# Kernel optimization log

Measured on AMD Instinct MI355X. Metric: run time of the kernel, lower is better.

Reference implementation:

```python
import jax, jax.numpy as jnp
import numpy as np

B, N, C_SA, OUT = 16, 2048, 512, 1024
BN_EPS = 1e-5


def pconv(x, w, b=None):
    # 1x1 Conv1d: x [B,Cin,N], w [Cout,Cin] -> [B,Cout,N]
    y = jnp.einsum('oc,bcn->bon', w, x)
    return y if b is None else y + b[None, :, None]


def setup_inputs() -> dict:
    key = jax.random.key(0)
    ks = jax.random.split(key, 16)
    s = lambda k, shape: jax.random.normal(k, shape, dtype=jnp.float32) * 0.05
    return {
        'x': jax.random.normal(ks[0], (B, 3, N), dtype=jnp.float32),
        'w1': s(ks[1], (128, 21)), 'b1': s(ks[2], (128,)),
        'w2': s(ks[3], (256, 128)), 'b2': s(ks[4], (256,)),
        'w3': s(ks[5], (512, 512)), 'b3': s(ks[6], (512,)),
        'w4': s(ks[7], (OUT, 512)), 'b4': s(ks[8], (OUT,)),
        'wqk': s(ks[9], (C_SA // 4, C_SA)),            # q_conv.weight tied to k_conv.weight, no bias
        'wv': s(ks[10], (C_SA, C_SA)), 'bv': s(ks[11], (C_SA,)),
        'wt': s(ks[12], (C_SA, C_SA)), 'bt': s(ks[13], (C_SA,)),
        'gamma': jnp.ones((C_SA,), dtype=jnp.float32),
        'beta': jnp.zeros((C_SA,), dtype=jnp.float32),
    }


def reference(x, w1, b1, w2, b2, w3, b3, w4, b4, wqk, wv, bv, wt, bt, gamma, beta):
    b, _, n = x.shape
    # positional encoding on [B,N,3]: [t, sin(t*2^i), cos(t*2^i)] for i in 0..2 -> 21 channels
    t = jnp.transpose(x, (0, 2, 1))
    enc = [t]
    for f in (1.0, 2.0, 4.0):
        enc.append(jnp.sin(t * f))
        enc.append(jnp.cos(t * f))
    h = jnp.transpose(jnp.concatenate(enc, axis=-1), (0, 2, 1))  # [B,21,N]

    h = jax.nn.relu(pconv(h, w1, b1))               # [B,128,N]
    h = pconv(h, w2, b2)                            # [B,256,N]
    g = jnp.max(h, axis=2)                          # [B,256]
    h = jnp.concatenate([h, jnp.broadcast_to(g[:, :, None], (b, g.shape[1], n))], axis=1)  # [B,512,N]
    h = jax.nn.relu(pconv(h, w3, b3))               # [B,512,N]

    # SA_Layer (offset attention, double normalization)
    xq = jnp.einsum('oc,bcn->bno', wqk, h)          # [B,N,128]
    xk = jnp.einsum('oc,bcn->bon', wqk, h)          # [B,128,N]
    xv = pconv(h, wv, bv)                           # [B,512,N]
    energy = jnp.einsum('bqo,bok->bqk', xq, xk)     # [B,N,N]
    attn = jax.nn.softmax(energy, axis=-1)
    attn = attn / (1e-9 + jnp.sum(attn, axis=1, keepdims=True))  # L1 renorm over query dim
    x_r = jnp.einsum('bck,bqk->bcq', xv, attn)      # x_v @ attn^T -> [B,512,N]
    d = pconv(h - x_r, wt, bt)
    # BatchNorm1d, training mode (batch statistics, biased variance)
    mu = jnp.mean(d, axis=(0, 2))
    var = jnp.var(d, axis=(0, 2))
    d = gamma[None, :, None] * (d - mu[None, :, None]) * jax.lax.rsqrt(var + BN_EPS)[None, :, None] + beta[None, :, None]
    h = h + jax.nn.relu(d)

    h = pconv(h, w4, b4)                            # [B,OUT,N]
    return jnp.max(h, axis=2)                       # [B,OUT]
```

## Files before the change

### kernel.cpp

```cpp
#include <hip/hip_runtime.h>
#include <cmath>

#define GN 2048
#define GB 16

typedef __attribute__((ext_vector_type(8))) short bf8_t;
typedef __attribute__((ext_vector_type(4))) float f4_t;

__device__ __forceinline__ short f2bf(float f) {
    union { float f; unsigned u; } v; v.f = f;
    unsigned r = v.u + 0x7FFFu + ((v.u >> 16) & 1u);
    return (short)(r >> 16);
}
__device__ __forceinline__ float bf2f(short s) {
    union { unsigned u; float f; } v; v.u = ((unsigned)(unsigned short)s) << 16;
    return v.f;
}

__device__ __forceinline__ void load16_lds(const short* g, short* l) {
    __builtin_amdgcn_global_load_lds(
        (const __attribute__((address_space(1))) unsigned int*)g,
        (__attribute__((address_space(3))) unsigned int*)l, 16, 0, 0);
}

__device__ __forceinline__ float wave_max(float v) {
#pragma unroll
    for (int o = 32; o > 0; o >>= 1) v = fmaxf(v, __shfl_xor(v, o, 64));
    return v;
}
__device__ __forceinline__ float wave_sum(float v) {
#pragma unroll
    for (int o = 32; o > 0; o >>= 1) v += __shfl_xor(v, o, 64);
    return v;
}
__device__ __forceinline__ float block_sum(float v) {
    __shared__ float sm[4];
    v = wave_sum(v);
    if ((threadIdx.x & 63) == 0) sm[threadIdx.x >> 6] = v;
    __syncthreads();
    v = sm[0] + sm[1] + sm[2] + sm[3];
    __syncthreads();
    return v;
}

__global__ __launch_bounds__(256) void f2ball_k(
    const float* __restrict__ w2, const float* __restrict__ w3,
    const float* __restrict__ wqk, const float* __restrict__ wv,
    const float* __restrict__ wt, const float* __restrict__ w4,
    short* __restrict__ dst) {
    int i = blockIdx.x * 256 + threadIdx.x;
    if (i >= 1409024) return;
    float v;
    if (i < 32768) v = w2[i];
    else if (i < 294912) v = w3[i - 32768];
    else if (i < 360448) v = wqk[i - 294912];
    else if (i < 622592) v = wv[i - 360448];
    else if (i < 884736) v = wt[i - 622592];
    else v = w4[i - 884736];
    dst[i] = f2bf(v);
}

__global__ __launch_bounds__(256) void posenc_conv1_k(
    const float* __restrict__ x, const float* __restrict__ w1,
    const float* __restrict__ b1, short* __restrict__ h1) {
    __shared__ float w[128 * 21];
    __shared__ float bb[128];
    __shared__ float se[256][21];
    const int tid = threadIdx.x;
    for (int i = tid; i < 128 * 21; i += 256) w[i] = w1[i];
    if (tid < 128) bb[tid] = b1[tid];
    int p0 = blockIdx.x * 256;
    int p = p0 + tid, b = p >> 11, n = p & (GN - 1);
    const float* xb = x + (long)b * 3 * GN + n;
    float t0 = xb[0], t1 = xb[GN], t2 = xb[2 * GN];
    se[tid][0] = t0; se[tid][1] = t1; se[tid][2] = t2;
    se[tid][3] = sinf(t0); se[tid][4] = sinf(t1); se[tid][5] = sinf(t2);
    se[tid][6] = cosf(t0); se[tid][7] = cosf(t1); se[tid][8] = cosf(t2);
    se[tid][9] = sinf(2.f * t0); se[tid][10] = sinf(2.f * t1); se[tid][11] = sinf(2.f * t2);
    se[tid][12] = cosf(2.f * t0); se[tid][13] = cosf(2.f * t1); se[tid][14] = cosf(2.f * t2);
    se[tid][15] = sinf(4.f * t0); se[tid][16] = sinf(4.f * t1); se[tid][17] = sinf(4.f * t2);
    se[tid][18] = cosf(4.f * t0); se[tid][19] = cosf(4.f * t1); se[tid][20] = cosf(4.f * t2);
    __syncthreads();
    short* outb = h1 + (long)p0 * 128;
    for (int it = 0; it < 128; ++it) {
        int L = it * 256 + tid;
        int pl = L >> 7, o = L & 127;
        float s = bb[o];
        const float* er = se[pl];
        const float* wr = &w[o * 21];
#pragma unroll
        for (int c = 0; c < 21; ++c) s = fmaf(wr[c], er[c], s);
        outb[L] = f2bf(fmaxf(s, 0.f));
    }
}

template <int MODE, int BIAS, bool RELU, bool STATS = false, bool COLMAX = false>
__global__ __launch_bounds__(256) void mm_k(
    const short* __restrict__ A, int lda, long long aB,
    const short* __restrict__ B, int ldb, long long bB,
    const float* __restrict__ bias, int biasStride,
    const short* __restrict__ aux, long long auxB,
    const float* __restrict__ rsv,
    float* __restrict__ Cf, long long cfB,
    short* __restrict__ Cb, long long cbB,
    float* __restrict__ Pmax, float* __restrict__ Ps2,
    int ldc, int K) {
    const int z = blockIdx.z;
    A += (long long)z * aB;
    B += (long long)z * bB;
    if (MODE == 4) { aux += (long long)z * auxB; rsv += (long long)z * GN; }
    if (MODE == 1) Cf += (long long)z * cfB;
    if (MODE == 2 || MODE == 4 || MODE == 6) Cb += (long long)z * cbB;
    if (MODE == 6) Pmax += (long long)z * GN * 32;
    const int row0 = blockIdx.x * 128, col0 = blockIdx.y * 128;
    const int tid = threadIdx.x;
    const int lane = tid & 63, w = tid >> 6;
    const int r = lane & 15, q = lane >> 4;
    const int wr = w >> 1, wc = w & 1;

    __shared__ short lA[8192];
    __shared__ short lB[8192];

    f4_t acc[4][4] = {};

    const int sRow = lane >> 2;
    const int sKb = (lane & 3) ^ ((lane >> 3) & 3);
    const long aG = (long)(row0 + w * 32 + sRow) * lda + sKb * 8;
    const long bG = (long)(col0 + w * 32 + sRow) * ldb + sKb * 8;
    short* ldsA0 = lA + (w * 32) * 32;
    short* ldsA1 = lA + (w * 32 + 16) * 32;
    short* ldsB0 = lB + (w * 32) * 32;
    short* ldsB1 = lB + (w * 32 + 16) * 32;

    const int sw = (q ^ ((r >> 1) & 3)) * 8;
    int aoff[4], boff[4];
#pragma unroll
    for (int i = 0; i < 4; ++i) {
        aoff[i] = (wr * 64 + i * 16 + r) * 32 + sw;
        boff[i] = (wc * 64 + i * 16 + r) * 32 + sw;
    }

    for (int k0 = 0; k0 < K; k0 += 64) {
        __syncthreads();
        load16_lds(A + aG + k0, ldsA0);
        load16_lds(A + aG + (long)16 * lda + k0, ldsA1);
        load16_lds(B + bG + k0, ldsB0);
        load16_lds(B + bG + (long)16 * ldb + k0, ldsB1);
        load16_lds(A + aG + k0 + 32, ldsA0 + 4096);
        load16_lds(A + aG + (long)16 * lda + k0 + 32, ldsA1 + 4096);
        load16_lds(B + bG + k0 + 32, ldsB0 + 4096);
        load16_lds(B + bG + (long)16 * ldb + k0 + 32, ldsB1 + 4096);
        asm volatile("s_waitcnt vmcnt(0)" ::: "memory");
        __syncthreads();
#pragma unroll
        for (int h = 0; h < 2; ++h) {
            const short* la = lA + h * 4096;
            const short* lb = lB + h * 4096;
            bf8_t av[4], bv[4];
#pragma unroll
            for (int i = 0; i < 4; ++i) av[i] = *(const bf8_t*)(la + aoff[i]);
#pragma unroll
            for (int j = 0; j < 4; ++j) bv[j] = *(const bf8_t*)(lb + boff[j]);
#pragma unroll
            for (int i = 0; i < 4; ++i)
#pragma unroll
                for (int j = 0; j < 4; ++j)
                    acc[i][j] = __builtin_amdgcn_mfma_f32_16x16x32_bf16(av[i], bv[j], acc[i][j], 0, 0, 0);
        }
    }

    if constexpr (MODE == 5) {
        int b = row0 >> 11;
        int rw = (blockIdx.x * 2 + wr) & 31;
#pragma unroll
        for (int j = 0; j < 4; ++j) {
            float vm = -1e30f;
#pragma unroll
            for (int i = 0; i < 4; ++i)
#pragma unroll
                for (int e = 0; e < 4; ++e) vm = fmaxf(vm, acc[i][j][e]);
            vm = fmaxf(vm, __shfl_xor(vm, 16, 64));
            vm = fmaxf(vm, __shfl_xor(vm, 32, 64));
            if (q == 0) {
                int gcol = col0 + wc * 64 + j * 16 + r;
                Pmax[(((long)b * 1024 + gcol) << 5) + rw] = vm + bias[gcol];
            }
        }
    } else if constexpr (MODE == 6) {
        float rsum[4][4] = {};
#pragma unroll
        for (int j = 0; j < 4; ++j) {
            int gcol = col0 + wc * 64 + j * 16 + r;
#pragma unroll
            for (int i = 0; i < 4; ++i) {
#pragma unroll
                for (int e = 0; e < 4; ++e) {
                    int grow = row0 + wr * 64 + i * 16 + q * 4 + e;
                    float ex = __expf(acc[i][j][e]);
                    rsum[i][e] += ex;
                    Cb[(long)grow * ldc + gcol] = f2bf(ex);
                }
            }
        }
#pragma unroll
        for (int i = 0; i < 4; ++i)
#pragma unroll
            for (int e = 0; e < 4; ++e) {
                float v = rsum[i][e];
                v += __shfl_xor(v, 1, 64);
                v += __shfl_xor(v, 2, 64);
                v += __shfl_xor(v, 4, 64);
                v += __shfl_xor(v, 8, 64);
                if (r == 0) {
                    int grow = row0 + wr * 64 + i * 16 + q * 4 + e;
                    Pmax[((long)grow << 5) + blockIdx.y * 2 + wc] = v;
                }
            }
    } else if constexpr (MODE == 4) {
#pragma unroll
        for (int i = 0; i < 4; ++i) {
#pragma unroll
            for (int e = 0; e < 4; ++e) {
                int grow = row0 + wr * 64 + i * 16 + q * 4 + e;
                float rsr = rsv[grow];
                long ob = (long)grow * ldc + col0 + wc * 64 + r;
#pragma unroll
                for (int j = 0; j < 4; ++j) {
                    long off = ob + j * 16;
                    Cb[off] = f2bf(bf2f(aux[off]) - acc[i][j][e] * rsr);
                }
            }
        }
    } else {
        const int b2d = (BIAS == 3) ? (row0 >> 11) : 0;
#pragma unroll
        for (int j = 0; j < 4; ++j) {
            int gcol = col0 + wc * 64 + j * 16 + r;
            float bvv = 0.f;
            if constexpr (BIAS == 1) bvv = bias[gcol];
            if constexpr (BIAS == 3) bvv = bias[b2d * biasStride + gcol];
            float s1 = 0.f, s2 = 0.f;
            float cmx = -1e30f;
#pragma unroll
            for (int i = 0; i < 4; ++i) {
#pragma unroll
                for (int e = 0; e < 4; ++e) {
                    int grow = row0 + wr * 64 + i * 16 + q * 4 + e;
                    float v = acc[i][j][e] + bvv;
                    if constexpr (BIAS == 2) v += bias[grow];
                    if constexpr (RELU) v = fmaxf(v, 0.f);
                    if constexpr (STATS) { s1 += v; s2 = fmaf(v, v, s2); }
                    if constexpr (COLMAX) cmx = fmaxf(cmx, v);
                    long off = (long)grow * ldc + gcol;
                    if constexpr (MODE == 1) Cf[off] = v;
                    if constexpr (MODE == 2) Cb[off] = f2bf(v);
                }
            }
            if constexpr (STATS) {
                s1 += __shfl_xor(s1, 16, 64); s1 += __shfl_xor(s1, 32, 64);
                s2 += __shfl_xor(s2, 16, 64); s2 += __shfl_xor(s2, 32, 64);
                if (q == 0) {
                    int rw2 = blockIdx.x * 2 + wr;
                    Pmax[rw2 * 512 + gcol] = s1;
                    Ps2[rw2 * 512 + gcol] = s2;
                }
            }
            if constexpr (COLMAX) {
                cmx = fmaxf(cmx, __shfl_xor(cmx, 16, 64));
                cmx = fmaxf(cmx, __shfl_xor(cmx, 32, 64));
                if (q == 0) {
                    int b = row0 >> 11;
                    int rw = (blockIdx.x * 2 + wr) & 31;
                    Pmax[(((long)b * ldc + gcol) << 5) + rw] = cmx;
                }
            }
        }
    }
}

__device__ __forceinline__ void stage2(const short* g0, const short* g1, short* dst) {
    load16_lds(g0, dst);
    load16_lds(g1, dst + 4096);
}

template <int MH, int NH>
__device__ __forceinline__ void mfma_quad(const bf8_t (&av)[4][2], const bf8_t (&bv)[2][2],
                                          f4_t (&acc)[8][4]) {
#pragma unroll
    for (int mi = 0; mi < 4; ++mi)
#pragma unroll
        for (int ni = 0; ni < 2; ++ni) {
            acc[MH * 4 + mi][NH * 2 + ni] = __builtin_amdgcn_mfma_f32_16x16x32_bf16(
                av[mi][0], bv[ni][0], acc[MH * 4 + mi][NH * 2 + ni], 0, 0, 0);
            acc[MH * 4 + mi][NH * 2 + ni] = __builtin_amdgcn_mfma_f32_16x16x32_bf16(
                av[mi][1], bv[ni][1], acc[MH * 4 + mi][NH * 2 + ni], 0, 0, 0);
        }
}

__device__ __forceinline__ void rd4(const short* p, int swz0, int swz1, bf8_t (&v)[4][2]) {
#pragma unroll
    for (int i = 0; i < 4; ++i) {
        v[i][0] = *(const bf8_t*)(p + i * 1024 + swz0);
        v[i][1] = *(const bf8_t*)(p + i * 1024 + swz1);
    }
}
__device__ __forceinline__ void rd2(const short* p, int swz0, int swz1, bf8_t (&v)[2][2]) {
#pragma unroll
    for (int i = 0; i < 2; ++i) {
        v[i][0] = *(const bf8_t*)(p + i * 1024 + swz0);
        v[i][1] = *(const bf8_t*)(p + i * 1024 + swz1);
    }
}

#define SB0 __builtin_amdgcn_sched_barrier(0)
#define BARRIER asm volatile("s_barrier" ::: "memory")

template <int MODE, int BIAS, bool RELU, bool STATS = false>
__global__ __launch_bounds__(512, 2) void mm256_k(
    const short* __restrict__ A, int lda, long long aB,
    const short* __restrict__ B, int ldb, long long bB,
    const float* __restrict__ bias,
    const short* __restrict__ aux, long long auxB,
    const float* __restrict__ rsv,
    short* __restrict__ Cb, long long cbB,
    float* __restrict__ Pmax, float* __restrict__ Ps2,
    int ldc, int K) {
    __shared__ short lA[32768];
    __shared__ short lB[32768];
    const int z = blockIdx.z;
    A += (long long)z * aB;
    B += (long long)z * bB;
    if constexpr (MODE == 4) { aux += (long long)z * auxB; rsv += (long long)z * GN; }
    if constexpr (MODE != 5) Cb += (long long)z * cbB;
    const int row0 = blockIdx.x * 256, col0 = blockIdx.y * 256;
    const int tid = threadIdx.x;
    const int lane = tid & 63, w = tid >> 6;
    const int r16 = lane & 15, q = lane >> 4;
    const int wr = w >> 2, wc = w & 3;

    const int rc0 = w * 8 + (lane >> 3);
    const int s8 = ((lane & 7) ^ (rc0 & 7)) * 8;
    const long ldA64 = (long)64 * lda, ldB64 = (long)64 * ldb;
    const short* aH0 = A + (long)(row0 + rc0) * lda + s8;
    const short* aH1 = aH0 + (long)128 * lda;
    const short* bH0 = B + (long)(col0 + rc0) * ldb + s8;
    const short* bH1 = bH0 + (long)128 * ldb;
    short* dA = lA + w * 512;
    short* dB = lB + w * 512;

#define STG_A(d_, h_, kt_) stage2((h_ ? aH1 : aH0) + (long)(kt_) * 64,                      \
                                  (h_ ? aH1 : aH0) + (long)(kt_) * 64 + ldA64,              \
                                  dA + (d_) * 16384 + (h_) * 8192)
#define STG_B(d_, h_, kt_) stage2((h_ ? bH1 : bH0) + (long)(kt_) * 64,                      \
                                  (h_ ? bH1 : bH0) + (long)(kt_) * 64 + ldB64,              \
                                  dB + (d_) * 16384 + (h_) * 8192)

    const int swz0 = (q ^ (r16 & 7)) * 8;
    const int swz1 = ((4 + q) ^ (r16 & 7)) * 8;
    const int arow = (wr * 64 + r16) * 64;
    const int brow = (wc * 32 + r16) * 64;

    f4_t acc[8][4] = {};
    bf8_t av[4][2], bv0[2][2], bv1[2][2];
    const int NT = K >> 6;

    STG_A(0, 0, 0); STG_B(0, 0, 0); STG_B(0, 1, 0); STG_A(0, 1, 0);
    STG_A(1, 0, 1); STG_B(1, 0, 1);
    asm volatile("s_waitcnt vmcnt(4)" ::: "memory");
    SB0; BARRIER; SB0;

    for (int t = 0; t < NT; ++t) {
        const int d = t & 1;
        const short* la = lA + d * 16384;
        const short* lb = lB + d * 16384;
        rd4(la + arow, swz0, swz1, av);
        rd2(lb + brow, swz0, swz1, bv0);
        if (t + 1 < NT) STG_B(d ^ 1, 1, t + 1);
        SB0; BARRIER; SB0;
        __builtin_amdgcn_s_setprio(1);
        mfma_quad<0, 0>(av, bv0, acc);
        __builtin_amdgcn_s_setprio(0);
        SB0; BARRIER; SB0;
        rd2(lb + 8192 + brow, swz0, swz1, bv1);
        if (t + 1 < NT) STG_A(d ^ 1, 1, t + 1);
        SB0; BARRIER; SB0;
        __builtin_amdgcn_s_setprio(1);
        mfma_quad<0, 1>(av, bv1, acc);
        __builtin_amdgcn_s_setprio(0);
        SB0; BARRIER; SB0;
        rd4(la + 8192 + arow, swz0, swz1, av);
        if (t + 2 < NT) STG_A(d, 0, t + 2);
        SB0; BARRIER; SB0;
        __builtin_amdgcn_s_setprio(1);
        mfma_quad<1, 0>(av, bv0, acc);
        __builtin_amdgcn_s_setprio(0);
        SB0; BARRIER; SB0;
        if (t + 2 < NT) {
            STG_B(d, 0, t + 2);
            asm volatile("s_waitcnt vmcnt(4)" ::: "memory");
        } else if (t + 1 < NT) {
            asm volatile("s_waitcnt vmcnt(0)" ::: "memory");
        }
        SB0; BARRIER; SB0;
        __builtin_amdgcn_s_setprio(1);
        mfma_quad<1, 1>(av, bv1, acc);
        __builtin_amdgcn_s_setprio(0);
        SB0; BARRIER; SB0;
    }
#undef STG_A
#undef STG_B

    const int mrow = row0 + wr * 64 + q * 4;
    const int ncol = col0 + wc * 32 + r16;

    if constexpr (MODE == 4) {
#pragma unroll
        for (int m = 0; m < 8; ++m) {
#pragma unroll
            for (int e = 0; e < 4; ++e) {
                const int grow = mrow + (m >> 2) * 128 + (m & 3) * 16 + e;
                const float rsr = rsv[grow];
                const long rb = (long)grow * ldc;
#pragma unroll
                for (int n = 0; n < 4; ++n) {
                    const long off = rb + ncol + (n >> 1) * 128 + (n & 1) * 16;
                    Cb[off] = f2bf(bf2f(aux[off]) - acc[m][n][e] * rsr);
                }
            }
        }
    } else if constexpr (MODE == 2) {
#pragma unroll
        for (int n = 0; n < 4; ++n) {
            const int gcol = ncol + (n >> 1) * 128 + (n & 1) * 16;
            float bvv = 0.f;
            if constexpr (BIAS == 1) bvv = bias[gcol];
#pragma unroll
            for (int mh = 0; mh < 2; ++mh) {
                float s1 = 0.f, s2 = 0.f;
#pragma unroll
                for (int mi = 0; mi < 4; ++mi) {
#pragma unroll
                    for (int e = 0; e < 4; ++e) {
                        const int grow = mrow + mh * 128 + mi * 16 + e;
                        float v = acc[mh * 4 + mi][n][e] + bvv;
                        if constexpr (RELU) v = fmaxf(v, 0.f);
                        if constexpr (STATS) { s1 += v; s2 = fmaf(v, v, s2); }
                        Cb[(long)grow * ldc + gcol] = f2bf(v);
                    }
                }
                if constexpr (STATS) {
                    s1 += __shfl_xor(s1, 16, 64); s1 += __shfl_xor(s1, 32, 64);
                    s2 += __shfl_xor(s2, 16, 64); s2 += __shfl_xor(s2, 32, 64);
                    if (q == 0) {
                        const int rw2 = blockIdx.x * 4 + mh * 2 + wr;
                        Pmax[rw2 * 512 + gcol] = s1;
                        Ps2[rw2 * 512 + gcol] = s2;
                    }
                }
            }
        }
    } else if constexpr (MODE == 5) {
        const int b = row0 >> 11;
#pragma unroll
        for (int n = 0; n < 4; ++n) {
            const int gcol = ncol + (n >> 1) * 128 + (n & 1) * 16;
            const float bvv = bias[gcol];
#pragma unroll
            for (int mh = 0; mh < 2; ++mh) {
                float vm = -1e30f;
#pragma unroll
                for (int mi = 0; mi < 4; ++mi)
#pragma unroll
                    for (int e = 0; e < 4; ++e) vm = fmaxf(vm, acc[mh * 4 + mi][n][e]);
                vm = fmaxf(vm, __shfl_xor(vm, 16, 64));
                vm = fmaxf(vm, __shfl_xor(vm, 32, 64));
                if (q == 0) {
                    const int rw = (blockIdx.x * 4 + mh * 2 + wr) & 31;
                    Pmax[(((long)b * ldc + gcol) << 5) + rw] = vm + bvv;
                }
            }
        }
    }
}
#undef SB0
#undef BARRIER

__global__ __launch_bounds__(256) void rs_k(const float* __restrict__ rp,
                                            float* __restrict__ rs) {
    int i = blockIdx.x * 256 + threadIdx.x;
    const float* p = rp + ((long)i << 5);
    float s = 0.f;
#pragma unroll
    for (int j = 0; j < 32; ++j) s += p[j];
    rs[i] = 1.f / s;
}

__global__ __launch_bounds__(256) void maxg_k(const float* __restrict__ P,
                                              float* __restrict__ g) {
    int i = blockIdx.x * 256 + threadIdx.x;
    const float* p = P + ((long)i << 5);
    float m = p[0];
#pragma unroll
    for (int j = 1; j < 32; ++j) m = fmaxf(m, p[j]);
    g[i] = m;
}

__global__ __launch_bounds__(256) void cvec_k(const float* __restrict__ w3,
                                              const float* __restrict__ b3,
                                              const float* __restrict__ g,
                                              float* __restrict__ cvec) {
    int idx = blockIdx.x * 256 + threadIdx.x;
    int b = idx >> 9, o = idx & 511;
    const float* gb = g + (b << 8);
    const float* wr = w3 + (long)o * 512 + 256;
    float s = b3[o];
    for (int c = 0; c < 256; ++c) s = fmaf(wr[c], gb[c], s);
    cvec[idx] = s;
}

__global__ __launch_bounds__(256) void colsum1_k(const short* __restrict__ Ab,
                                                 const float* __restrict__ rs,
                                                 float* __restrict__ cp) {
    int kb = blockIdx.x, qs = blockIdx.y, z = blockIdx.z;
    int k = kb * 256 + threadIdx.x;
    const short* p = Ab + (long)z * GN * GN + (long)qs * 64 * GN + k;
    const float* rv = rs + z * GN + qs * 64;
    float s = 0.f;
    for (int qq = 0; qq < 64; ++qq) s += bf2f(p[(long)qq * GN]) * rv[qq];
    cp[((z * 32 + qs) * GN) + k] = s;
}
__global__ __launch_bounds__(256) void colsum2_k(const float* __restrict__ cp,
                                                 float* __restrict__ cs) {
    int k = blockIdx.x * 256 + threadIdx.x, z = blockIdx.y;
    float s = 1e-9f;
    for (int qs = 0; qs < 32; ++qs) s += cp[((z * 32 + qs) * GN) + k];
    cs[z * GN + k] = s;
}

__global__ __launch_bounds__(256) void xvscale_k(short* __restrict__ xvc,
                                                 const float* __restrict__ cs) {
    long idx = ((long)blockIdx.x * 256 + threadIdx.x) * 4;
    int p = (int)(idx & 32767);
    short* ptr = xvc + idx;
    float4 cv = *(const float4*)(cs + p);
    uint2 u = *(const uint2*)ptr;
    short* sp = (short*)&u;
    sp[0] = f2bf(bf2f(sp[0]) / cv.x);
    sp[1] = f2bf(bf2f(sp[1]) / cv.y);
    sp[2] = f2bf(bf2f(sp[2]) / cv.z);
    sp[3] = f2bf(bf2f(sp[3]) / cv.w);
    *(uint2*)ptr = u;
}

__global__ __launch_bounds__(256) void bn2_k(const float* __restrict__ bs1,
                                             const float* __restrict__ bs2,
                                             const float* __restrict__ gamma,
                                             const float* __restrict__ beta,
                                             float* __restrict__ sc,
                                             float* __restrict__ sh) {
    int c = blockIdx.x;
    float s = 0.f, s2 = 0.f;
    for (int i = threadIdx.x; i < 512; i += 256) {
        s += bs1[i * 512 + c];
        s2 += bs2[i * 512 + c];
    }
    s = block_sum(s);
    s2 = block_sum(s2);
    if (threadIdx.x == 0) {
        const float cnt = (float)(GB * GN);
        float mu = s / cnt;
        float var = s2 / cnt - mu * mu;
        float r = rsqrtf(var + 1e-5f);
        float gm = gamma[c] * r;
        sc[c] = gm;
        sh[c] = beta[c] - gm * mu;
    }
}

__global__ __launch_bounds__(256) void bn_apply_k(const short* __restrict__ h3b,
                                                  const short* __restrict__ d,
                                                  const float* __restrict__ sc,
                                                  const float* __restrict__ sh,
                                                  short* __restrict__ h4) {
    long bidx = ((long)blockIdx.x * 256 + threadIdx.x) * 4;
    int c = (int)(bidx & 511);
    uint2 du = *(const uint2*)(d + bidx);
    short* ds = (short*)&du;
    uint2 hu = *(const uint2*)(h3b + bidx);
    short* hs = (short*)&hu;
    float4 a4 = *(const float4*)(sc + c);
    float4 b4 = *(const float4*)(sh + c);
    float r0 = bf2f(hs[0]) + fmaxf(fmaf(bf2f(ds[0]), a4.x, b4.x), 0.f);
    float r1 = bf2f(hs[1]) + fmaxf(fmaf(bf2f(ds[1]), a4.y, b4.y), 0.f);
    float r2 = bf2f(hs[2]) + fmaxf(fmaf(bf2f(ds[2]), a4.z, b4.z), 0.f);
    float r3 = bf2f(hs[3]) + fmaxf(fmaf(bf2f(ds[3]), a4.w, b4.w), 0.f);
    uint2 o;
    o.x = (unsigned short)f2bf(r0) | ((unsigned)(unsigned short)f2bf(r1) << 16);
    o.y = (unsigned short)f2bf(r2) | ((unsigned)(unsigned short)f2bf(r3) << 16);
    *(uint2*)(h4 + bidx) = o;
}

__global__ __launch_bounds__(256) void max_final_k(const float* __restrict__ P,
                                                   float* __restrict__ out) {
    int i = blockIdx.x * 256 + threadIdx.x;
    const float* p = P + ((long)i << 5);
    float m = p[0];
#pragma unroll
    for (int j = 1; j < 32; ++j) m = fmaxf(m, p[j]);
    out[i] = m;
}

extern "C" void kernel_launch(void* const* d_in, const int* in_sizes, int n_in,
                              void* d_out, int out_size, void* d_ws, size_t ws_size,
                              hipStream_t stream) {
    const float* x = (const float*)d_in[0];
    const float* w1 = (const float*)d_in[1];
    const float* b1 = (const float*)d_in[2];
    const float* w2 = (const float*)d_in[3];
    const float* b2 = (const float*)d_in[4];
    const float* w3 = (const float*)d_in[5];
    const float* b3 = (const float*)d_in[6];
    const float* w4 = (const float*)d_in[7];
    const float* b4 = (const float*)d_in[8];
    const float* wqk = (const float*)d_in[9];
    const float* wv = (const float*)d_in[10];
    const float* bv = (const float*)d_in[11];
    const float* wt = (const float*)d_in[12];
    const float* bt = (const float*)d_in[13];
    const float* gamma = (const float*)d_in[14];
    const float* beta = (const float*)d_in[15];
    float* out = (float*)d_out;

    char* base = (char*)d_ws;
    short* h3b = (short*)base;
    short* hsT = (short*)(base + 33554432);
    short* kT  = (short*)(base + 67108864);
    short* xvc = (short*)(base + 75497472);
    short* EA  = (short*)(base + 109051904);
    short* h1T = (short*)(base + 109051904);
    short* h2T = (short*)(base + 117440512);
    short* dTb = (short*)(base + 109051904);
    short* h4T = (short*)(base + 67108864);
    char* S = base + 243269632;
    float* g    = (float*)(S + 262144);
    float* cvec = (float*)(S + 278528);
    float* cp   = (float*)(S + 311296);
    float* rp   = cp;
    float* cs   = (float*)(S + 4505600);
    float* bs1  = (float*)(S + 4636672);
    float* bs2  = (float*)(S + 5685248);
    float* bnsc = (float*)(S + 6733824);
    float* bnsh = (float*)(S + 6735872);
    float* Pmax = (float*)(S + 6737920);
    short* w2b  = (short*)(S + 8835072);
    short* w3b  = (short*)(S + 8900608);
    short* wqkb = (short*)(S + 9424896);
    short* wvb  = (short*)(S + 9555968);
    short* wtb  = (short*)(S + 10080256);
    short* w4b  = (short*)(S + 10604544);
    float* rs   = (float*)(S + 11653120);

    f2ball_k<<<5505, 256, 0, stream>>>(w2, w3, wqk, wv, wt, w4, w2b);

    posenc_conv1_k<<<128, 256, 0, stream>>>(x, w1, b1, h1T);

    mm_k<2, 1, false, false, true><<<dim3(256, 2, 1), 256, 0, stream>>>(
        h1T, 128, 0, w2b, 128, 0, b2, 0, nullptr, 0, nullptr,
        nullptr, 0, h2T, 0, Pmax, nullptr, 256, 128);

    maxg_k<<<16, 256, 0, stream>>>(Pmax, g);

    cvec_k<<<32, 256, 0, stream>>>(w3, b3, g, cvec);

    mm_k<2, 3, true><<<dim3(256, 4, 1), 256, 0, stream>>>(
        h2T, 256, 0, w3b, 512, 0, cvec, 512, nullptr, 0, nullptr,
        nullptr, 0, h3b, 0, nullptr, nullptr, 512, 256);

    mm_k<2, 0, false><<<dim3(256, 1, 1), 256, 0, stream>>>(
        h3b, 512, 0, wqkb, 512, 0, nullptr, 0, nullptr, 0, nullptr,
        nullptr, 0, kT, 0, nullptr, nullptr, 128, 512);

    mm_k<2, 2, false><<<dim3(4, 256, 1), 256, 0, stream>>>(
        wvb, 512, 0, h3b, 512, 0, bv, 0, nullptr, 0, nullptr,
        nullptr, 0, xvc, 0, nullptr, nullptr, 32768, 512);

    mm_k<6, 0, false><<<dim3(16, 16, 16), 256, 0, stream>>>(
        kT, 128, (long long)GN * 128, kT, 128, (long long)GN * 128,
        nullptr, 0, nullptr, 0, nullptr, nullptr, 0,
        EA, (long long)GN * GN, rp, nullptr, GN, 128);
    rs_k<<<128, 256, 0, stream>>>(rp, rs);
    colsum1_k<<<dim3(8, 32, GB), 256, 0, stream>>>(EA, rs, cp);
    colsum2_k<<<dim3(8, GB), 256, 0, stream>>>(cp, cs);
    xvscale_k<<<16384, 256, 0, stream>>>(xvc, cs);
    mm256_k<4, 0, false><<<dim3(8, 2, 16), 512, 0, stream>>>(
        EA, GN, (long long)GN * GN,
        xvc, 32768, (long long)GN,
        nullptr, h3b, (long long)GN * 512, rs,
        hsT, (long long)GN * 512, nullptr, nullptr, 512, GN);

    mm256_k<2, 1, false, true><<<dim3(128, 2, 1), 512, 0, stream>>>(
        hsT, 512, 0, wtb, 512, 0, bt, nullptr, 0, nullptr,
        dTb, 0, bs1, bs2, 512, 512);

    bn2_k<<<512, 256, 0, stream>>>(bs1, bs2, gamma, beta, bnsc, bnsh);

    bn_apply_k<<<16384, 256, 0, stream>>>(h3b, dTb, bnsc, bnsh, h4T);

    mm256_k<5, 1, false><<<dim3(128, 4, 1), 512, 0, stream>>>(
        h4T, 512, 0, w4b, 512, 0, b4, nullptr, 0, nullptr,
        nullptr, 0, Pmax, nullptr, 1024, 512);

    max_final_k<<<64, 256, 0, stream>>>(Pmax, out);
}
```

Measured before the change: 467.7 us.

## Move conv3 and value GEMMs to 256-tile kernel, swizzle attention grid, vectorize colsum

The conv3 and value-projection GEMMs now use the 256x256, 512-thread mm256_k kernel instead of the smaller mm_k. To support this, mm256_k gains per-batch bias (BIAS==3) and per-row bias (BIAS==2) modes. The attention x_v GEMM gets an XCD-aware block-index swizzle so neighbouring workgroups land on the same chiplet and share L2. colsum1 is rewritten so each thread reads eight bf16 values per 16-byte load. Together these aim to improve data reuse and memory efficiency, at the cost of fewer, larger blocks and possible occupancy changes.

```diff
diff --git a/kernel.cpp b/kernel.cpp
--- a/kernel.cpp
+++ b/kernel.cpp
@@ -315,11 +315,11 @@
 #define SB0 __builtin_amdgcn_sched_barrier(0)
 #define BARRIER asm volatile("s_barrier" ::: "memory")
 
-template <int MODE, int BIAS, bool RELU, bool STATS = false>
+template <int MODE, int BIAS, bool RELU, bool STATS = false, bool SWZ = false>
 __global__ __launch_bounds__(512, 2) void mm256_k(
     const short* __restrict__ A, int lda, long long aB,
     const short* __restrict__ B, int ldb, long long bB,
-    const float* __restrict__ bias,
+    const float* __restrict__ bias, int biasStride,
     const short* __restrict__ aux, long long auxB,
     const float* __restrict__ rsv,
     short* __restrict__ Cb, long long cbB,
@@ -327,12 +327,23 @@
     int ldc, int K) {
     __shared__ short lA[32768];
     __shared__ short lB[32768];
-    const int z = blockIdx.z;
+    int bx = blockIdx.x, by = blockIdx.y, bz = blockIdx.z;
+    if constexpr (SWZ) {
+        const int nwg = gridDim.x * gridDim.y * gridDim.z;
+        const int bid = bx + gridDim.x * (by + gridDim.y * bz);
+        const int cpx = nwg >> 3;
+        const int wg = (bid & 7) * cpx + (bid >> 3);
+        bx = wg % gridDim.x;
+        const int t2 = wg / gridDim.x;
+        by = t2 % gridDim.y;
+        bz = t2 / gridDim.y;
+    }
+    const int z = bz;
     A += (long long)z * aB;
     B += (long long)z * bB;
     if constexpr (MODE == 4) { aux += (long long)z * auxB; rsv += (long long)z * GN; }
     if constexpr (MODE != 5) Cb += (long long)z * cbB;
-    const int row0 = blockIdx.x * 256, col0 = blockIdx.y * 256;
+    const int row0 = bx * 256, col0 = by * 256;
     const int tid = threadIdx.x;
     const int lane = tid & 63, w = tid >> 6;
     const int r16 = lane & 15, q = lane >> 4;
@@ -429,11 +440,13 @@
             }
         }
     } else if constexpr (MODE == 2) {
+        const int b2d = (BIAS == 3) ? (row0 >> 11) : 0;
 #pragma unroll
         for (int n = 0; n < 4; ++n) {
             const int gcol = ncol + (n >> 1) * 128 + (n & 1) * 16;
             float bvv = 0.f;
             if constexpr (BIAS == 1) bvv = bias[gcol];
+            if constexpr (BIAS == 3) bvv = bias[b2d * biasStride + gcol];
 #pragma unroll
             for (int mh = 0; mh < 2; ++mh) {
                 float s1 = 0.f, s2 = 0.f;
@@ -443,6 +456,7 @@
                     for (int e = 0; e < 4; ++e) {
                         const int grow = mrow + mh * 128 + mi * 16 + e;
                         float v = acc[mh * 4 + mi][n][e] + bvv;
+                        if constexpr (BIAS == 2) v += bias[grow];
                         if constexpr (RELU) v = fmaxf(v, 0.f);
                         if constexpr (STATS) { s1 += v; s2 = fmaf(v, v, s2); }
                         Cb[(long)grow * ldc + gcol] = f2bf(v);
@@ -452,7 +466,7 @@
                     s1 += __shfl_xor(s1, 16, 64); s1 += __shfl_xor(s1, 32, 64);
                     s2 += __shfl_xor(s2, 16, 64); s2 += __shfl_xor(s2, 32, 64);
                     if (q == 0) {
-                        const int rw2 = blockIdx.x * 4 + mh * 2 + wr;
+                        const int rw2 = bx * 4 + mh * 2 + wr;
                         Pmax[rw2 * 512 + gcol] = s1;
                         Ps2[rw2 * 512 + gcol] = s2;
                     }
@@ -475,7 +489,7 @@
                 vm = fmaxf(vm, __shfl_xor(vm, 16, 64));
                 vm = fmaxf(vm, __shfl_xor(vm, 32, 64));
                 if (q == 0) {
-                    const int rw = (blockIdx.x * 4 + mh * 2 + wr) & 31;
+                    const int rw = (bx * 4 + mh * 2 + wr) & 31;
                     Pmax[(((long)b * ldc + gcol) << 5) + rw] = vm + bvv;
                 }
             }
@@ -521,13 +535,21 @@
 __global__ __launch_bounds__(256) void colsum1_k(const short* __restrict__ Ab,
                                                  const float* __restrict__ rs,
                                                  float* __restrict__ cp) {
-    int kb = blockIdx.x, qs = blockIdx.y, z = blockIdx.z;
-    int k = kb * 256 + threadIdx.x;
-    const short* p = Ab + (long)z * GN * GN + (long)qs * 64 * GN + k;
+    const int qs = blockIdx.x, z = blockIdx.y;
+    const int k0 = threadIdx.x * 8;
+    const short* p = Ab + (long)z * GN * GN + (long)qs * 64 * GN + k0;
     const float* rv = rs + z * GN + qs * 64;
-    float s = 0.f;
-    for (int qq = 0; qq < 64; ++qq) s += bf2f(p[(long)qq * GN]) * rv[qq];
-    cp[((z * 32 + qs) * GN) + k] = s;
+    float s[8] = {};
+    for (int qq = 0; qq < 64; ++qq) {
+        uint4 v = *(const uint4*)(p + (long)qq * GN);
+        const float rr = rv[qq];
+        const short* sp = (const short*)&v;
+#pragma unroll
+        for (int j = 0; j < 8; ++j) s[j] = fmaf(bf2f(sp[j]), rr, s[j]);
+    }
+    float* o = cp + ((long)(z * 32 + qs) * GN) + k0;
+#pragma unroll
+    for (int j = 0; j < 8; ++j) o[j] = s[j];
 }
 __global__ __launch_bounds__(256) void colsum2_k(const float* __restrict__ cp,
                                                  float* __restrict__ cs) {
@@ -672,34 +694,34 @@
 
     cvec_k<<<32, 256, 0, stream>>>(w3, b3, g, cvec);
 
-    mm_k<2, 3, true><<<dim3(256, 4, 1), 256, 0, stream>>>(
+    mm256_k<2, 3, true><<<dim3(128, 2, 1), 512, 0, stream>>>(
         h2T, 256, 0, w3b, 512, 0, cvec, 512, nullptr, 0, nullptr,
-        nullptr, 0, h3b, 0, nullptr, nullptr, 512, 256);
+        h3b, 0, nullptr, nullptr, 512, 256);
 
     mm_k<2, 0, false><<<dim3(256, 1, 1), 256, 0, stream>>>(
         h3b, 512, 0, wqkb, 512, 0, nullptr, 0, nullptr, 0, nullptr,
         nullptr, 0, kT, 0, nullptr, nullptr, 128, 512);
 
-    mm_k<2, 2, false><<<dim3(4, 256, 1), 256, 0, stream>>>(
+    mm256_k<2, 2, false><<<dim3(2, 128, 1), 512, 0, stream>>>(
         wvb, 512, 0, h3b, 512, 0, bv, 0, nullptr, 0, nullptr,
-        nullptr, 0, xvc, 0, nullptr, nullptr, 32768, 512);
+        xvc, 0, nullptr, nullptr, 32768, 512);
 
     mm_k<6, 0, false><<<dim3(16, 16, 16), 256, 0, stream>>>(
         kT, 128, (long long)GN * 128, kT, 128, (long long)GN * 128,
         nullptr, 0, nullptr, 0, nullptr, nullptr, 0,
         EA, (long long)GN * GN, rp, nullptr, GN, 128);
     rs_k<<<128, 256, 0, stream>>>(rp, rs);
-    colsum1_k<<<dim3(8, 32, GB), 256, 0, stream>>>(EA, rs, cp);
+    colsum1_k<<<dim3(32, GB), 256, 0, stream>>>(EA, rs, cp);
     colsum2_k<<<dim3(8, GB), 256, 0, stream>>>(cp, cs);
     xvscale_k<<<16384, 256, 0, stream>>>(xvc, cs);
-    mm256_k<4, 0, false><<<dim3(8, 2, 16), 512, 0, stream>>>(
+    mm256_k<4, 0, false, false, true><<<dim3(8, 2, 16), 512, 0, stream>>>(
         EA, GN, (long long)GN * GN,
         xvc, 32768, (long long)GN,
-        nullptr, h3b, (long long)GN * 512, rs,
+        nullptr, 0, h3b, (long long)GN * 512, rs,
         hsT, (long long)GN * 512, nullptr, nullptr, 512, GN);
 
     mm256_k<2, 1, false, true><<<dim3(128, 2, 1), 512, 0, stream>>>(
-        hsT, 512, 0, wtb, 512, 0, bt, nullptr, 0, nullptr,
+        hsT, 512, 0, wtb, 512, 0, bt, 0, nullptr, 0, nullptr,
         dTb, 0, bs1, bs2, 512, 512);
 
     bn2_k<<<512, 256, 0, stream>>>(bs1, bs2, gamma, beta, bnsc, bnsh);
@@ -707,7 +729,7 @@
     bn_apply_k<<<16384, 256, 0, stream>>>(h3b, dTb, bnsc, bnsh, h4T);
 
     mm256_k<5, 1, false><<<dim3(128, 4, 1), 512, 0, stream>>>(
-        h4T, 512, 0, w4b, 512, 0, b4, nullptr, 0, nullptr,
+        h4T, 512, 0, w4b, 512, 0, b4, 0, nullptr, 0, nullptr,
         nullptr, 0, Pmax, nullptr, 1024, 512);
 
     max_final_k<<<64, 256, 0, stream>>>(Pmax, out);
```

Result: no change. 476.5 us (+1.9%).
